# Performance work log

Hardware: AMD Instinct MI355X
Metric: run time of the kernel (lower is better)

Reference implementation:

```python
import jax, jax.numpy as jnp
import numpy as np

ROPE_BASE = 100.0  # CroCo/InfiniteVGGT-style 2D RoPE base

def _rope_1d(sub, pos, base=ROPE_BASE):
    # sub: (B,H,N,half), pos: (B,N) float
    half = sub.shape[-1]
    quarter = half // 2
    inv_freq = 1.0 / (base ** (jnp.arange(quarter, dtype=jnp.float32) / quarter))
    ang = pos[:, None, :, None] * inv_freq  # (B,1,N,quarter)
    cos, sin = jnp.cos(ang), jnp.sin(ang)
    x1, x2 = sub[..., :quarter], sub[..., quarter:]
    return jnp.concatenate([x1 * cos - x2 * sin, x1 * sin + x2 * cos], axis=-1)

def rope_2d(t, positions):
    # t: (B,H,N,Dh); positions: (B,N,2) int (y,x)
    Dh = t.shape[-1]
    half = Dh // 2
    pos_f = positions.astype(t.dtype)
    y = _rope_1d(t[..., :half], pos_f[..., 0])
    x = _rope_1d(t[..., half:], pos_f[..., 1])
    return jnp.concatenate([y, x], axis=-1)

def setup_inputs() -> dict:
    key = jax.random.key(0)
    k1, k2, k3, k4 = jax.random.split(key, 4)
    B, N, C, H = 2, 2048, 1024, 16
    x = jax.random.normal(k1, (B, N, C), dtype=jnp.float32)
    positions = jax.random.randint(k2, (B, N, 2), 0, 64, dtype=jnp.int32)
    qkv_w = jax.random.normal(k3, (3 * C, C), dtype=jnp.float32) * (C ** -0.5)
    proj_w = jax.random.normal(k4, (C, C), dtype=jnp.float32) * (C ** -0.5)
    proj_b = jnp.zeros((C,), dtype=jnp.float32)
    return {"x": x, "positions": positions, "qkv_w": qkv_w, "proj_w": proj_w, "proj_b": proj_b}

def reference(x, positions, qkv_w, proj_w, proj_b):
    B, N, C = x.shape
    H = 16
    Dh = C // H
    scale = Dh ** -0.5
    qkv = (x @ qkv_w.T).reshape(B, N, 3, H, Dh).transpose(2, 0, 3, 1, 4)  # (3,B,H,N,Dh)
    q, k, v = qkv[0], qkv[1], qkv[2]
    q = rope_2d(q, positions)
    k = rope_2d(k, positions)
    attn = jnp.einsum('bhnd,bhmd->bhnm', q, k) * scale  # (B,H,N,N)
    attn = jax.nn.softmax(attn, axis=-1)
    out = jnp.einsum('bhnm,bhmd->bhnd', attn, v)  # (B,H,N,Dh)
    out = out.transpose(0, 2, 1, 3).reshape(B, N, C)
    return out @ proj_w.T + proj_b
```

## Files before the change

### kernel.cpp

```cpp
#include <hip/hip_runtime.h>
#include <cmath>

typedef unsigned short u16;
typedef unsigned int   u32;
typedef __attribute__((ext_vector_type(8))) __bf16 bf16x8;
typedef __attribute__((ext_vector_type(2))) __bf16 bf16x2;
typedef __attribute__((ext_vector_type(4))) float  f32x4;

constexpr int BB = 2, SEQ = 2048, CH = 1024, NH = 16, DH = 64;

__device__ inline u16 f2bf(float f) {
    u32 u = __builtin_bit_cast(u32, f);
    u += 0x7FFF + ((u >> 16) & 1);
    return (u16)(u >> 16);
}
__device__ inline float bf2f(u16 b) { return __builtin_bit_cast(float, (u32)b << 16); }
__device__ inline u32 pkbf(float a, float b) {
#if __has_builtin(__builtin_amdgcn_cvt_pk_bf16_f32)
    bf16x2 r = __builtin_amdgcn_cvt_pk_bf16_f32(a, b);
    return __builtin_bit_cast(u32, r);
#else
    return (u32)f2bf(a) | ((u32)f2bf(b) << 16);
#endif
}
__device__ inline float fexp2(float x) {
#if __has_builtin(__builtin_amdgcn_exp2f)
    return __builtin_amdgcn_exp2f(x);
#else
    return exp2f(x);
#endif
}

__device__ inline void gld_lds16(const void* g, void* l) {
    __builtin_amdgcn_global_load_lds((const __attribute__((address_space(1))) void*)g,
                                     (__attribute__((address_space(3))) void*)l, 16, 0, 0);
}
__device__ inline f32x4 mfma16(bf16x8 a, bf16x8 b, f32x4 c) {
    return __builtin_amdgcn_mfma_f32_16x16x32_bf16(a, b, c, 0, 0, 0);
}
__device__ inline bf16x8 ld_frag(const u16* p) {
    return __builtin_bit_cast(bf16x8, *(const uint4*)p);
}

__global__ __launch_bounds__(256) void convert_kernel(const float* __restrict__ x,
                                                      const float* __restrict__ wq,
                                                      const float* __restrict__ wp,
                                                      u16* __restrict__ xb,
                                                      u16* __restrict__ wqb,
                                                      u16* __restrict__ wpb,
                                                      float2* __restrict__ tabq,
                                                      float2* __restrict__ tabk) {
    const int q = blockIdx.x * 256 + threadIdx.x;
    if (q >= 2097152) {
        const int idx = q - 2097152;
        if (idx < 1024) {
            const int p = idx >> 4, i = idx & 15;
            const float f = exp2f(-(float)i * 0.41524101186092f);
            float s, c;
            sincosf((float)p * f, &s, &c);
            tabk[idx] = make_float2(c, s);
            tabq[idx] = make_float2(c * 0.18033688011112042f,
                                    s * 0.18033688011112042f);
        }
        return;
    }
    const float* src; u16* dst; int idx;
    if (q < 1048576)            { src = x;  dst = xb;  idx = q; }
    else if (q < 1048576+786432){ src = wq; dst = wqb; idx = q - 1048576; }
    else                        { src = wp; dst = wpb; idx = q - 1048576 - 786432; }
    float4 v = *(const float4*)(src + (size_t)idx * 4);
    ushort4 o; o.x = f2bf(v.x); o.y = f2bf(v.y); o.z = f2bf(v.z); o.w = f2bf(v.w);
    *(ushort4*)(dst + (size_t)idx * 4) = o;
}

__global__ __launch_bounds__(256) void gemm_qkv_rope(const u16* __restrict__ A,
                                                     const u16* __restrict__ Bw,
                                                     const int* __restrict__ pos,
                                                     const float2* __restrict__ tabq,
                                                     const float2* __restrict__ tabk,
                                                     u16* __restrict__ Qb,
                                                     u16* __restrict__ Kb,
                                                     u16* __restrict__ Vt) {
    __shared__ u16 smem[18432];
    const int t = threadIdx.x, lane = t & 63, w = t >> 6;
    const int l15 = lane & 15, quad = lane >> 4;
    const int wm = w >> 1, wn = w & 1;
    const int m0 = blockIdx.y * 128, n0 = blockIdx.x * 128;
    const int K = CH;

    const int row0 = t >> 2, v0 = t & 3;
    const int gi0 = (v0 - (row0 >> 1)) & 3;
    const int row1 = row0 + 64;
    const int gi1 = (v0 - (row1 >> 1)) & 3;

    const u16* A0 = A  + (size_t)(m0 + row0) * K + gi0 * 8;
    const u16* A1 = A  + (size_t)(m0 + row1) * K + gi1 * 8;
    const u16* B0 = Bw + (size_t)(n0 + row0) * K + gi0 * 8;
    const u16* B1 = Bw + (size_t)(n0 + row1) * K + gi1 * 8;

    gld_lds16(A0, smem + t * 8);
    gld_lds16(A1, smem + 2048 + t * 8);
    gld_lds16(B0, smem + 8192 + t * 8);
    gld_lds16(B1, smem + 10240 + t * 8);

    f32x4 acc[4][4] = {};
    for (int kt = 0; kt < K / 32; ++kt) {
        __syncthreads();
        const int cur = (kt & 1) * 4096;
        if (kt + 1 < K / 32) {
            const int off = (kt + 1) * 32;
            const int nxt = ((kt + 1) & 1) * 4096;
            gld_lds16(A0 + off, smem + nxt + t * 8);
            gld_lds16(A1 + off, smem + nxt + 2048 + t * 8);
            gld_lds16(B0 + off, smem + 8192 + nxt + t * 8);
            gld_lds16(B1 + off, smem + 8192 + nxt + 2048 + t * 8);
        }
        const u16* as = smem + cur;
        const u16* bs = smem + 8192 + cur;
        bf16x8 af[4], bfv[4];
#pragma unroll
        for (int mi = 0; mi < 4; ++mi) {
            const int r = wm * 64 + mi * 16 + l15;
            af[mi] = ld_frag(as + (r * 4 + ((quad + (r >> 1)) & 3)) * 8);
        }
#pragma unroll
        for (int nj = 0; nj < 4; ++nj) {
            const int r = wn * 64 + nj * 16 + l15;
            bfv[nj] = ld_frag(bs + (r * 4 + ((quad + (r >> 1)) & 3)) * 8);
        }
#pragma unroll
        for (int mi = 0; mi < 4; ++mi)
#pragma unroll
            for (int nj = 0; nj < 4; ++nj)
                acc[mi][nj] = mfma16(af[mi], bfv[nj], acc[mi][nj]);
    }

    const int reg = n0 >> 10;
    const int h   = ((n0 & 1023) >> 6) + wn;
    if (reg < 2) {
        const float2* tab = reg ? tabk : tabq;
        u16* dst = reg ? Kb : Qb;
#pragma unroll
        for (int mi = 0; mi < 4; ++mi) {
#pragma unroll
            for (int r = 0; r < 4; ++r) {
                const int m = m0 + wm * 64 + mi * 16 + quad * 4 + r;
                const int bh = (m >> 11) * NH + h;
                const int n  = m & 2047;
                const int2 pp = *(const int2*)(pos + m * 2);
                const float2 ty = tab[pp.x * 16 + l15];
                const float2 tx = tab[pp.y * 16 + l15];
                const float x1 = acc[mi][0][r], x2 = acc[mi][1][r];
                const float y1 = acc[mi][2][r], y2 = acc[mi][3][r];
                u16* p = dst + ((size_t)bh * SEQ + n) * 64 + l15;
                p[0]  = f2bf(x1 * ty.x - x2 * ty.y);
                p[16] = f2bf(x1 * ty.y + x2 * ty.x);
                p[32] = f2bf(y1 * tx.x - y2 * tx.y);
                p[48] = f2bf(y1 * tx.y + y2 * tx.x);
            }
        }
    } else {
        __syncthreads();
        u16* T = smem + w * 4608;
#pragma unroll
        for (int mi = 0; mi < 4; ++mi)
#pragma unroll
            for (int nj = 0; nj < 4; ++nj)
#pragma unroll
                for (int r = 0; r < 4; ++r)
                    T[(nj * 16 + l15) * 72 + mi * 16 + quad * 4 + r] =
                        f2bf(acc[mi][nj][r]);
        const int bh = (m0 >> 11) * NH + h;
        const int nbase = (m0 & 2047) + wm * 64;
        u16* gdst = Vt + ((size_t)bh * 64 + lane) * SEQ + nbase;
#pragma unroll
        for (int j = 0; j < 8; ++j)
            *(uint4*)(gdst + j * 8) = *(const uint4*)(T + lane * 72 + j * 8);
    }
}

__global__ __launch_bounds__(256) void gemm_bf16(const u16* __restrict__ A,
                                                 const u16* __restrict__ Bw,
                                                 const float* __restrict__ bias,
                                                 float* __restrict__ C,
                                                 int M, int N, int K) {
    __shared__ u16 smem[16384];
    const int t = threadIdx.x, lane = t & 63, w = t >> 6;
    const int l15 = lane & 15, quad = lane >> 4;
    const int wm = w >> 1, wn = w & 1;
    const int m0 = blockIdx.y * 128, n0 = blockIdx.x * 128;

    const int row0 = t >> 2, v0 = t & 3;
    const int gi0 = (v0 - (row0 >> 1)) & 3;
    const int row1 = row0 + 64;
    const int gi1 = (v0 - (row1 >> 1)) & 3;

    const u16* A0 = A  + (size_t)(m0 + row0) * K + gi0 * 8;
    const u16* A1 = A  + (size_t)(m0 + row1) * K + gi1 * 8;
    const u16* B0 = Bw + (size_t)(n0 + row0) * K + gi0 * 8;
    const u16* B1 = Bw + (size_t)(n0 + row1) * K + gi1 * 8;

    gld_lds16(A0, smem + t * 8);
    gld_lds16(A1, smem + 2048 + t * 8);
    gld_lds16(B0, smem + 8192 + t * 8);
    gld_lds16(B1, smem + 10240 + t * 8);

    f32x4 acc[4][4] = {};
    for (int kt = 0; kt < K / 32; ++kt) {
        __syncthreads();
        const int cur = (kt & 1) * 4096;
        if (kt + 1 < K / 32) {
            const int off = (kt + 1) * 32;
            const int nxt = ((kt + 1) & 1) * 4096;
            gld_lds16(A0 + off, smem + nxt + t * 8);
            gld_lds16(A1 + off, smem + nxt + 2048 + t * 8);
            gld_lds16(B0 + off, smem + 8192 + nxt + t * 8);
            gld_lds16(B1 + off, smem + 8192 + nxt + 2048 + t * 8);
        }
        const u16* as = smem + cur;
        const u16* bs = smem + 8192 + cur;
        bf16x8 af[4], bfv[4];
#pragma unroll
        for (int mi = 0; mi < 4; ++mi) {
            const int r = wm * 64 + mi * 16 + l15;
            af[mi] = ld_frag(as + (r * 4 + ((quad + (r >> 1)) & 3)) * 8);
        }
#pragma unroll
        for (int nj = 0; nj < 4; ++nj) {
            const int r = wn * 64 + nj * 16 + l15;
            bfv[nj] = ld_frag(bs + (r * 4 + ((quad + (r >> 1)) & 3)) * 8);
        }
#pragma unroll
        for (int mi = 0; mi < 4; ++mi)
#pragma unroll
            for (int nj = 0; nj < 4; ++nj)
                acc[mi][nj] = mfma16(af[mi], bfv[nj], acc[mi][nj]);
    }
#pragma unroll
    for (int mi = 0; mi < 4; ++mi)
#pragma unroll
        for (int nj = 0; nj < 4; ++nj) {
            const int n = n0 + wn * 64 + nj * 16 + l15;
            const float bv = bias[n];
#pragma unroll
            for (int r = 0; r < 4; ++r) {
                const int m = m0 + wm * 64 + mi * 16 + quad * 4 + r;
                C[(size_t)m * N + n] = acc[mi][nj][r] + bv;
            }
        }
}

__global__ __launch_bounds__(256, 4) void attn_mfma(const u16* __restrict__ Qb,
                                                    const u16* __restrict__ Kb,
                                                    const u16* __restrict__ Vt,
                                                    u16* __restrict__ Opart,
                                                    float* __restrict__ lpart) {
    __shared__ u16 Ks[64 * 64];
    __shared__ u16 Vs[64 * 64];
    __shared__ u16 Ps[128 * 72];
    const int t = threadIdx.x, lane = t & 63, w = t >> 6;
    const int l15 = lane & 15, quad = lane >> 4;
    const int bh = blockIdx.y;
    const int q0 = blockIdx.x * 128;
    const int z  = blockIdx.z;

    const int rowA = t >> 3, vA = t & 7;
    const int giA = (vA - rowA) & 7;
    const int rowB = rowA + 32;
    const int giB = (vA - rowB) & 7;

    const size_t kbase = (size_t)bh * SEQ * 64;
    const size_t vbase = (size_t)bh * 64 * SEQ;

    const uint4 ones_u = {0x3F803F80u, 0x3F803F80u, 0x3F803F80u, 0x3F803F80u};
    const bf16x8 onesf = __builtin_bit_cast(bf16x8, ones_u);

    bf16x8 aq[2][2];
#pragma unroll
    for (int mi = 0; mi < 2; ++mi)
#pragma unroll
        for (int ks = 0; ks < 2; ++ks)
            aq[mi][ks] = ld_frag(Qb + ((size_t)bh * SEQ + q0 + w * 32 + mi * 16 + l15) * 64
                                 + ks * 32 + quad * 8);

    f32x4 oacc[2][4] = {};
    f32x4 lacc[2] = {};

    for (int kt = 0; kt < 16; ++kt) {
        const int k0 = z * 1024 + kt * 64;
        __syncthreads();
        gld_lds16(Kb + kbase + (size_t)(k0 + rowA) * 64 + giA * 8, Ks + t * 8);
        gld_lds16(Kb + kbase + (size_t)(k0 + rowB) * 64 + giB * 8, Ks + 2048 + t * 8);
        gld_lds16(Vt + vbase + (size_t)rowA * SEQ + k0 + giA * 8, Vs + t * 8);
        gld_lds16(Vt + vbase + (size_t)rowB * SEQ + k0 + giB * 8, Vs + 2048 + t * 8);
        __syncthreads();

        f32x4 sacc[2][4] = {};
#pragma unroll
        for (int ks = 0; ks < 2; ++ks)
#pragma unroll
            for (int nk = 0; nk < 4; ++nk) {
                const int rK = nk * 16 + l15;
                const bf16x8 kf = ld_frag(Ks + (rK * 8 + (((ks * 4 + quad) + rK) & 7)) * 8);
                sacc[0][nk] = mfma16(kf, aq[0][ks], sacc[0][nk]);
                sacc[1][nk] = mfma16(kf, aq[1][ks], sacc[1][nk]);
            }

#pragma unroll
        for (int mi = 0; mi < 2; ++mi) {
            const int prow = (w * 32 + mi * 16 + l15) * 72;
#pragma unroll
            for (int nk = 0; nk < 4; ++nk) {
                const float p0 = fexp2(sacc[mi][nk][0]);
                const float p1 = fexp2(sacc[mi][nk][1]);
                const float p2 = fexp2(sacc[mi][nk][2]);
                const float p3 = fexp2(sacc[mi][nk][3]);
                uint2 pk; pk.x = pkbf(p0, p1); pk.y = pkbf(p2, p3);
                *(uint2*)&Ps[prow + nk * 16 + quad * 4] = pk;
            }
        }

#pragma unroll
        for (int ks = 0; ks < 2; ++ks) {
            const bf16x8 ap0 = ld_frag(Ps + (w * 32 + l15) * 72 + ks * 32 + quad * 8);
            const bf16x8 ap1 = ld_frag(Ps + (w * 32 + 16 + l15) * 72 + ks * 32 + quad * 8);
            lacc[0] = mfma16(ap0, onesf, lacc[0]);
            lacc[1] = mfma16(ap1, onesf, lacc[1]);
#pragma unroll
            for (int nj = 0; nj < 4; ++nj) {
                const int rV = nj * 16 + l15;
                const bf16x8 vf = ld_frag(Vs + (rV * 8 + (((ks * 4 + quad) + rV) & 7)) * 8);
                oacc[0][nj] = mfma16(ap0, vf, oacc[0][nj]);
                oacc[1][nj] = mfma16(ap1, vf, oacc[1][nj]);
            }
        }
    }

#pragma unroll
    for (int mi = 0; mi < 2; ++mi)
#pragma unroll
        for (int r = 0; r < 4; ++r) {
            const int qrow = q0 + w * 32 + mi * 16 + quad * 4 + r;
            if (l15 == 0)
                lpart[((size_t)z * 32 + bh) * SEQ + qrow] = lacc[mi][r];
            const size_t orow = (((size_t)z * 32 + bh) * SEQ + qrow) * 64;
#pragma unroll
            for (int nj = 0; nj < 4; ++nj)
                Opart[orow + nj * 16 + l15] = f2bf(oacc[mi][nj][r]);
        }
}

__global__ __launch_bounds__(256) void merge_kernel(const u16* __restrict__ Opart,
                                                    const float* __restrict__ lpart,
                                                    u16* __restrict__ Ob) {
    const int gid = blockIdx.x * 256 + threadIdx.x;
    const int d4 = gid & 15, q = (gid >> 4) & 2047, bh = gid >> 15;
    const size_t i1 = ((size_t)bh * SEQ + q) * 64 + d4 * 4;
    const size_t i2 = i1 + (size_t)32 * SEQ * 64;
    const float inv = 1.0f / (lpart[(size_t)bh * SEQ + q] +
                              lpart[(size_t)(32 + bh) * SEQ + q]);
    const ushort4 a = *(const ushort4*)(Opart + i1);
    const ushort4 b = *(const ushort4*)(Opart + i2);
    ushort4 o;
    o.x = f2bf((bf2f(a.x) + bf2f(b.x)) * inv);
    o.y = f2bf((bf2f(a.y) + bf2f(b.y)) * inv);
    o.z = f2bf((bf2f(a.z) + bf2f(b.z)) * inv);
    o.w = f2bf((bf2f(a.w) + bf2f(b.w)) * inv);
    const int b_ = bh >> 4, h = bh & 15;
    *(ushort4*)(Ob + ((size_t)(b_ * SEQ + q)) * CH + h * 64 + d4 * 4) = o;
}

extern "C" void kernel_launch(void* const* d_in, const int* in_sizes, int n_in,
                              void* d_out, int out_size, void* d_ws, size_t ws_size,
                              hipStream_t stream) {
    const float* x      = (const float*)d_in[0];
    const int*   pos    = (const int*)d_in[1];
    const float* qkv_w  = (const float*)d_in[2];
    const float* proj_w = (const float*)d_in[3];
    const float* proj_b = (const float*)d_in[4];
    float* out = (float*)d_out;

    u16* ws = (u16*)d_ws;
    u16* x_bf    = ws;
    u16* attn_bf = ws;
    u16* wq_bf   = ws + 4194304;
    float* lpart = (float*)(ws + 4194304);
    u16* wp_bf   = ws + 7340032;
    u16* Qb      = ws + 8388608;
    u16* Kb      = ws + 12582912;
    u16* Vt      = ws + 16777216;
    u16* Opart   = ws + 20971520;
    float2* tabq = (float2*)(ws + 20971520);
    float2* tabk = (float2*)(ws + 20971520 + 4096);

    const int M = BB * SEQ;

    convert_kernel<<<8196, 256, 0, stream>>>(x, qkv_w, proj_w, x_bf, wq_bf, wp_bf,
                                             tabq, tabk);
    gemm_qkv_rope<<<dim3(3 * CH / 128, M / 128), 256, 0, stream>>>(
        x_bf, wq_bf, pos, tabq, tabk, Qb, Kb, Vt);
    attn_mfma<<<dim3(SEQ / 128, BB * NH, 2), 256, 0, stream>>>(Qb, Kb, Vt, Opart, lpart);
    merge_kernel<<<4096, 256, 0, stream>>>(Opart, lpart, attn_bf);
    gemm_bf16<<<dim3(CH / 128, M / 128), 256, 0, stream>>>(
        attn_bf, wp_bf, proj_b, out, M, CH, CH);
}
```

Baseline: 201.6 us.

## Drop attention split-K merge, double-buffer KV, split-K proj GEMM with atomics

The QKV GEMM epilogue now stages RoPE'd Q/K through LDS and writes coalesced 16-byte rows, and V's transpose store is remapped so lanes write contiguous chunks. Attention no longer splits the key range in two. Each block walks all 2048 keys with double-buffered K/V LDS tiles, normalises in-kernel and writes the final bf16 output directly. This removes the merge kernel and the partial-output traffic, but halves the attention grid and drops the occupancy hint. The projection GEMM is split into two K halves that accumulate into a zero-initialised output with float atomics. This adds parallelism at the cost of a memset and atomic traffic.

```diff
diff --git a/kernel.cpp b/kernel.cpp
--- a/kernel.cpp
+++ b/kernel.cpp
@@ -137,31 +137,39 @@
 
     const int reg = n0 >> 10;
     const int h   = ((n0 & 1023) >> 6) + wn;
+    __syncthreads();
+    u16* T = smem + w * 4608;
+    const int rsel = lane >> 3, csel = lane & 7;
     if (reg < 2) {
         const float2* tab = reg ? tabk : tabq;
-        u16* dst = reg ? Kb : Qb;
+        u16* dstb = reg ? Kb : Qb;
 #pragma unroll
         for (int mi = 0; mi < 4; ++mi) {
 #pragma unroll
             for (int r = 0; r < 4; ++r) {
                 const int m = m0 + wm * 64 + mi * 16 + quad * 4 + r;
-                const int bh = (m >> 11) * NH + h;
-                const int n  = m & 2047;
                 const int2 pp = *(const int2*)(pos + m * 2);
                 const float2 ty = tab[pp.x * 16 + l15];
                 const float2 tx = tab[pp.y * 16 + l15];
                 const float x1 = acc[mi][0][r], x2 = acc[mi][1][r];
                 const float y1 = acc[mi][2][r], y2 = acc[mi][3][r];
-                u16* p = dst + ((size_t)bh * SEQ + n) * 64 + l15;
-                p[0]  = f2bf(x1 * ty.x - x2 * ty.y);
-                p[16] = f2bf(x1 * ty.y + x2 * ty.x);
-                p[32] = f2bf(y1 * tx.x - y2 * tx.y);
-                p[48] = f2bf(y1 * tx.y + y2 * tx.x);
+                const int ml = (mi * 16 + quad * 4 + r) * 72;
+                T[ml + l15]      = f2bf(x1 * ty.x - x2 * ty.y);
+                T[ml + l15 + 16] = f2bf(x1 * ty.y + x2 * ty.x);
+                T[ml + l15 + 32] = f2bf(y1 * tx.x - y2 * tx.y);
+                T[ml + l15 + 48] = f2bf(y1 * tx.y + y2 * tx.x);
             }
         }
+        const int mbase = m0 + wm * 64;
+        const int bh = (mbase >> 11) * NH + h;
+        const int nbase = mbase & 2047;
+#pragma unroll
+        for (int j = 0; j < 8; ++j) {
+            const int row = rsel + j * 8;
+            u16* gp = dstb + ((size_t)bh * SEQ + nbase + row) * 64 + csel * 8;
+            *(uint4*)gp = *(const uint4*)&T[row * 72 + csel * 8];
+        }
     } else {
-        __syncthreads();
-        u16* T = smem + w * 4608;
 #pragma unroll
         for (int mi = 0; mi < 4; ++mi)
 #pragma unroll
@@ -172,105 +180,36 @@
                         f2bf(acc[mi][nj][r]);
         const int bh = (m0 >> 11) * NH + h;
         const int nbase = (m0 & 2047) + wm * 64;
-        u16* gdst = Vt + ((size_t)bh * 64 + lane) * SEQ + nbase;
-#pragma unroll
-        for (int j = 0; j < 8; ++j)
-            *(uint4*)(gdst + j * 8) = *(const uint4*)(T + lane * 72 + j * 8);
+#pragma unroll
+        for (int j = 0; j < 8; ++j) {
+            const int d = rsel + j * 8;
+            u16* gp = Vt + ((size_t)bh * 64 + d) * SEQ + nbase + csel * 8;
+            *(uint4*)gp = *(const uint4*)&T[d * 72 + csel * 8];
+        }
     }
 }
 
-__global__ __launch_bounds__(256) void gemm_bf16(const u16* __restrict__ A,
-                                                 const u16* __restrict__ Bw,
-                                                 const float* __restrict__ bias,
-                                                 float* __restrict__ C,
-                                                 int M, int N, int K) {
-    __shared__ u16 smem[16384];
-    const int t = threadIdx.x, lane = t & 63, w = t >> 6;
-    const int l15 = lane & 15, quad = lane >> 4;
-    const int wm = w >> 1, wn = w & 1;
-    const int m0 = blockIdx.y * 128, n0 = blockIdx.x * 128;
-
-    const int row0 = t >> 2, v0 = t & 3;
-    const int gi0 = (v0 - (row0 >> 1)) & 3;
-    const int row1 = row0 + 64;
-    const int gi1 = (v0 - (row1 >> 1)) & 3;
-
-    const u16* A0 = A  + (size_t)(m0 + row0) * K + gi0 * 8;
-    const u16* A1 = A  + (size_t)(m0 + row1) * K + gi1 * 8;
-    const u16* B0 = Bw + (size_t)(n0 + row0) * K + gi0 * 8;
-    const u16* B1 = Bw + (size_t)(n0 + row1) * K + gi1 * 8;
-
-    gld_lds16(A0, smem + t * 8);
-    gld_lds16(A1, smem + 2048 + t * 8);
-    gld_lds16(B0, smem + 8192 + t * 8);
-    gld_lds16(B1, smem + 10240 + t * 8);
-
-    f32x4 acc[4][4] = {};
-    for (int kt = 0; kt < K / 32; ++kt) {
-        __syncthreads();
-        const int cur = (kt & 1) * 4096;
-        if (kt + 1 < K / 32) {
-            const int off = (kt + 1) * 32;
-            const int nxt = ((kt + 1) & 1) * 4096;
-            gld_lds16(A0 + off, smem + nxt + t * 8);
-            gld_lds16(A1 + off, smem + nxt + 2048 + t * 8);
-            gld_lds16(B0 + off, smem + 8192 + nxt + t * 8);
-            gld_lds16(B1 + off, smem + 8192 + nxt + 2048 + t * 8);
-        }
-        const u16* as = smem + cur;
-        const u16* bs = smem + 8192 + cur;
-        bf16x8 af[4], bfv[4];
-#pragma unroll
-        for (int mi = 0; mi < 4; ++mi) {
-            const int r = wm * 64 + mi * 16 + l15;
-            af[mi] = ld_frag(as + (r * 4 + ((quad + (r >> 1)) & 3)) * 8);
-        }
-#pragma unroll
-        for (int nj = 0; nj < 4; ++nj) {
-            const int r = wn * 64 + nj * 16 + l15;
-            bfv[nj] = ld_frag(bs + (r * 4 + ((quad + (r >> 1)) & 3)) * 8);
-        }
-#pragma unroll
-        for (int mi = 0; mi < 4; ++mi)
-#pragma unroll
-            for (int nj = 0; nj < 4; ++nj)
-                acc[mi][nj] = mfma16(af[mi], bfv[nj], acc[mi][nj]);
-    }
-#pragma unroll
-    for (int mi = 0; mi < 4; ++mi)
-#pragma unroll
-        for (int nj = 0; nj < 4; ++nj) {
-            const int n = n0 + wn * 64 + nj * 16 + l15;
-            const float bv = bias[n];
-#pragma unroll
-            for (int r = 0; r < 4; ++r) {
-                const int m = m0 + wm * 64 + mi * 16 + quad * 4 + r;
-                C[(size_t)m * N + n] = acc[mi][nj][r] + bv;
-            }
-        }
-}
-
-__global__ __launch_bounds__(256, 4) void attn_mfma(const u16* __restrict__ Qb,
-                                                    const u16* __restrict__ Kb,
-                                                    const u16* __restrict__ Vt,
-                                                    u16* __restrict__ Opart,
-                                                    float* __restrict__ lpart) {
-    __shared__ u16 Ks[64 * 64];
-    __shared__ u16 Vs[64 * 64];
+__global__ __launch_bounds__(256) void attn_mfma(const u16* __restrict__ Qb,
+                                                 const u16* __restrict__ Kb,
+                                                 const u16* __restrict__ Vt,
+                                                 u16* __restrict__ Ob) {
+    __shared__ u16 Ks[2][4096];
+    __shared__ u16 Vs[2][4096];
     __shared__ u16 Ps[128 * 72];
     const int t = threadIdx.x, lane = t & 63, w = t >> 6;
     const int l15 = lane & 15, quad = lane >> 4;
     const int bh = blockIdx.y;
     const int q0 = blockIdx.x * 128;
-    const int z  = blockIdx.z;
 
     const int rowA = t >> 3, vA = t & 7;
     const int giA = (vA - rowA) & 7;
     const int rowB = rowA + 32;
     const int giB = (vA - rowB) & 7;
 
-    const size_t kbase = (size_t)bh * SEQ * 64;
-    const size_t vbase = (size_t)bh * 64 * SEQ;
+    const u16* Ksrc0 = Kb + (size_t)bh * SEQ * 64 + (size_t)rowA * 64 + giA * 8;
+    const u16* Ksrc1 = Kb + (size_t)bh * SEQ * 64 + (size_t)rowB * 64 + giB * 8;
+    const u16* Vsrc0 = Vt + (size_t)bh * 64 * SEQ + (size_t)rowA * SEQ + giA * 8;
+    const u16* Vsrc1 = Vt + (size_t)bh * 64 * SEQ + (size_t)rowB * SEQ + giB * 8;
 
     const uint4 ones_u = {0x3F803F80u, 0x3F803F80u, 0x3F803F80u, 0x3F803F80u};
     const bf16x8 onesf = __builtin_bit_cast(bf16x8, ones_u);
@@ -286,14 +225,21 @@
     f32x4 oacc[2][4] = {};
     f32x4 lacc[2] = {};
 
-    for (int kt = 0; kt < 16; ++kt) {
-        const int k0 = z * 1024 + kt * 64;
+    gld_lds16(Ksrc0, &Ks[0][t * 8]);
+    gld_lds16(Ksrc1, &Ks[0][t * 8 + 2048]);
+    gld_lds16(Vsrc0, &Vs[0][t * 8]);
+    gld_lds16(Vsrc1, &Vs[0][t * 8 + 2048]);
+
+    for (int kt = 0; kt < 32; ++kt) {
         __syncthreads();
-        gld_lds16(Kb + kbase + (size_t)(k0 + rowA) * 64 + giA * 8, Ks + t * 8);
-        gld_lds16(Kb + kbase + (size_t)(k0 + rowB) * 64 + giB * 8, Ks + 2048 + t * 8);
-        gld_lds16(Vt + vbase + (size_t)rowA * SEQ + k0 + giA * 8, Vs + t * 8);
-        gld_lds16(Vt + vbase + (size_t)rowB * SEQ + k0 + giB * 8, Vs + 2048 + t * 8);
-        __syncthreads();
+        const int cur = kt & 1;
+        if (kt + 1 < 32) {
+            const int nxt = cur ^ 1;
+            gld_lds16(Ksrc0 + (kt + 1) * 4096, &Ks[nxt][t * 8]);
+            gld_lds16(Ksrc1 + (kt + 1) * 4096, &Ks[nxt][t * 8 + 2048]);
+            gld_lds16(Vsrc0 + (kt + 1) * 64,   &Vs[nxt][t * 8]);
+            gld_lds16(Vsrc1 + (kt + 1) * 64,   &Vs[nxt][t * 8 + 2048]);
+        }
 
         f32x4 sacc[2][4] = {};
 #pragma unroll
@@ -301,7 +247,8 @@
 #pragma unroll
             for (int nk = 0; nk < 4; ++nk) {
                 const int rK = nk * 16 + l15;
-                const bf16x8 kf = ld_frag(Ks + (rK * 8 + (((ks * 4 + quad) + rK) & 7)) * 8);
+                const bf16x8 kf =
+                    ld_frag(&Ks[cur][(rK * 8 + (((ks * 4 + quad) + rK) & 7)) * 8]);
                 sacc[0][nk] = mfma16(kf, aq[0][ks], sacc[0][nk]);
                 sacc[1][nk] = mfma16(kf, aq[1][ks], sacc[1][nk]);
             }
@@ -322,52 +269,106 @@
 
 #pragma unroll
         for (int ks = 0; ks < 2; ++ks) {
-            const bf16x8 ap0 = ld_frag(Ps + (w * 32 + l15) * 72 + ks * 32 + quad * 8);
-            const bf16x8 ap1 = ld_frag(Ps + (w * 32 + 16 + l15) * 72 + ks * 32 + quad * 8);
+            const bf16x8 ap0 = ld_frag(&Ps[(w * 32 + l15) * 72 + ks * 32 + quad * 8]);
+            const bf16x8 ap1 = ld_frag(&Ps[(w * 32 + 16 + l15) * 72 + ks * 32 + quad * 8]);
             lacc[0] = mfma16(ap0, onesf, lacc[0]);
             lacc[1] = mfma16(ap1, onesf, lacc[1]);
 #pragma unroll
             for (int nj = 0; nj < 4; ++nj) {
                 const int rV = nj * 16 + l15;
-                const bf16x8 vf = ld_frag(Vs + (rV * 8 + (((ks * 4 + quad) + rV) & 7)) * 8);
+                const bf16x8 vf =
+                    ld_frag(&Vs[cur][(rV * 8 + (((ks * 4 + quad) + rV) & 7)) * 8]);
                 oacc[0][nj] = mfma16(ap0, vf, oacc[0][nj]);
                 oacc[1][nj] = mfma16(ap1, vf, oacc[1][nj]);
             }
         }
     }
 
+    const int b_ = bh >> 4, h = bh & 15;
 #pragma unroll
     for (int mi = 0; mi < 2; ++mi)
 #pragma unroll
         for (int r = 0; r < 4; ++r) {
+            const float inv = 1.0f / lacc[mi][r];
             const int qrow = q0 + w * 32 + mi * 16 + quad * 4 + r;
-            if (l15 == 0)
-                lpart[((size_t)z * 32 + bh) * SEQ + qrow] = lacc[mi][r];
-            const size_t orow = (((size_t)z * 32 + bh) * SEQ + qrow) * 64;
+            u16* op = Ob + ((size_t)(b_ * SEQ + qrow)) * CH + h * 64;
 #pragma unroll
             for (int nj = 0; nj < 4; ++nj)
-                Opart[orow + nj * 16 + l15] = f2bf(oacc[mi][nj][r]);
-        }
-}
-
-__global__ __launch_bounds__(256) void merge_kernel(const u16* __restrict__ Opart,
-                                                    const float* __restrict__ lpart,
-                                                    u16* __restrict__ Ob) {
-    const int gid = blockIdx.x * 256 + threadIdx.x;
-    const int d4 = gid & 15, q = (gid >> 4) & 2047, bh = gid >> 15;
-    const size_t i1 = ((size_t)bh * SEQ + q) * 64 + d4 * 4;
-    const size_t i2 = i1 + (size_t)32 * SEQ * 64;
-    const float inv = 1.0f / (lpart[(size_t)bh * SEQ + q] +
-                              lpart[(size_t)(32 + bh) * SEQ + q]);
-    const ushort4 a = *(const ushort4*)(Opart + i1);
-    const ushort4 b = *(const ushort4*)(Opart + i2);
-    ushort4 o;
-    o.x = f2bf((bf2f(a.x) + bf2f(b.x)) * inv);
-    o.y = f2bf((bf2f(a.y) + bf2f(b.y)) * inv);
-    o.z = f2bf((bf2f(a.z) + bf2f(b.z)) * inv);
-    o.w = f2bf((bf2f(a.w) + bf2f(b.w)) * inv);
-    const int b_ = bh >> 4, h = bh & 15;
-    *(ushort4*)(Ob + ((size_t)(b_ * SEQ + q)) * CH + h * 64 + d4 * 4) = o;
+                op[nj * 16 + l15] = f2bf(oacc[mi][nj][r] * inv);
+        }
+}
+
+__global__ __launch_bounds__(256) void gemm_proj(const u16* __restrict__ A,
+                                                 const u16* __restrict__ Bw,
+                                                 const float* __restrict__ bias,
+                                                 float* __restrict__ C) {
+    __shared__ u16 smem[16384];
+    const int t = threadIdx.x, lane = t & 63, w = t >> 6;
+    const int l15 = lane & 15, quad = lane >> 4;
+    const int wm = w >> 1, wn = w & 1;
+    const int m0 = blockIdx.y * 128, n0 = blockIdx.x * 128;
+    const int K = CH, N = CH;
+    const int k0 = blockIdx.z * 512;
+
+    const int row0 = t >> 2, v0 = t & 3;
+    const int gi0 = (v0 - (row0 >> 1)) & 3;
+    const int row1 = row0 + 64;
+    const int gi1 = (v0 - (row1 >> 1)) & 3;
+
+    const u16* A0 = A  + (size_t)(m0 + row0) * K + k0 + gi0 * 8;
+    const u16* A1 = A  + (size_t)(m0 + row1) * K + k0 + gi1 * 8;
+    const u16* B0 = Bw + (size_t)(n0 + row0) * K + k0 + gi0 * 8;
+    const u16* B1 = Bw + (size_t)(n0 + row1) * K + k0 + gi1 * 8;
+
+    gld_lds16(A0, smem + t * 8);
+    gld_lds16(A1, smem + 2048 + t * 8);
+    gld_lds16(B0, smem + 8192 + t * 8);
+    gld_lds16(B1, smem + 10240 + t * 8);
+
+    f32x4 acc[4][4] = {};
+    for (int kt = 0; kt < 16; ++kt) {
+        __syncthreads();
+        const int cur = (kt & 1) * 4096;
+        if (kt + 1 < 16) {
+            const int off = (kt + 1) * 32;
+            const int nxt = ((kt + 1) & 1) * 4096;
+            gld_lds16(A0 + off, smem + nxt + t * 8);
+            gld_lds16(A1 + off, smem + nxt + 2048 + t * 8);
+            gld_lds16(B0 + off, smem + 8192 + nxt + t * 8);
+            gld_lds16(B1 + off, smem + 8192 + nxt + 2048 + t * 8);
+        }
+        const u16* as = smem + cur;
+        const u16* bs = smem + 8192 + cur;
+        bf16x8 af[4], bfv[4];
+#pragma unroll
+        for (int mi = 0; mi < 4; ++mi) {
+            const int r = wm * 64 + mi * 16 + l15;
+            af[mi] = ld_frag(as + (r * 4 + ((quad + (r >> 1)) & 3)) * 8);
+        }
+#pragma unroll
+        for (int nj = 0; nj < 4; ++nj) {
+            const int r = wn * 64 + nj * 16 + l15;
+            bfv[nj] = ld_frag(bs + (r * 4 + ((quad + (r >> 1)) & 3)) * 8);
+        }
+#pragma unroll
+        for (int mi = 0; mi < 4; ++mi)
+#pragma unroll
+            for (int nj = 0; nj < 4; ++nj)
+                acc[mi][nj] = mfma16(af[mi], bfv[nj], acc[mi][nj]);
+    }
+    const int addb = (blockIdx.z == 0);
+#pragma unroll
+    for (int mi = 0; mi < 4; ++mi)
+#pragma unroll
+        for (int nj = 0; nj < 4; ++nj) {
+            const int n = n0 + wn * 64 + nj * 16 + l15;
+            const float bv = addb ? bias[n] : 0.0f;
+#pragma unroll
+            for (int r = 0; r < 4; ++r) {
+                const int m = m0 + wm * 64 + mi * 16 + quad * 4 + r;
+                atomicAdd(&C[(size_t)m * N + n], acc[mi][nj][r] + bv);
+            }
+        }
 }
 
 extern "C" void kernel_launch(void* const* d_in, const int* in_sizes, int n_in,
@@ -384,23 +385,21 @@
     u16* x_bf    = ws;
     u16* attn_bf = ws;
     u16* wq_bf   = ws + 4194304;
-    float* lpart = (float*)(ws + 4194304);
     u16* wp_bf   = ws + 7340032;
     u16* Qb      = ws + 8388608;
     u16* Kb      = ws + 12582912;
     u16* Vt      = ws + 16777216;
-    u16* Opart   = ws + 20971520;
     float2* tabq = (float2*)(ws + 20971520);
     float2* tabk = (float2*)(ws + 20971520 + 4096);
 
     const int M = BB * SEQ;
 
+    hipMemsetAsync(out, 0, (size_t)out_size * sizeof(float), stream);
     convert_kernel<<<8196, 256, 0, stream>>>(x, qkv_w, proj_w, x_bf, wq_bf, wp_bf,
                                              tabq, tabk);
     gemm_qkv_rope<<<dim3(3 * CH / 128, M / 128), 256, 0, stream>>>(
         x_bf, wq_bf, pos, tabq, tabk, Qb, Kb, Vt);
-    attn_mfma<<<dim3(SEQ / 128, BB * NH, 2), 256, 0, stream>>>(Qb, Kb, Vt, Opart, lpart);
-    merge_kernel<<<4096, 256, 0, stream>>>(Opart, lpart, attn_bf);
-    gemm_bf16<<<dim3(CH / 128, M / 128), 256, 0, stream>>>(
-        attn_bf, wp_bf, proj_b, out, M, CH, CH);
-}
+    attn_mfma<<<dim3(SEQ / 128, BB * NH), 256, 0, stream>>>(Qb, Kb, Vt, attn_bf);
+    gemm_proj<<<dim3(CH / 128, M / 128, 2), 256, 0, stream>>>(
+        attn_bf, wp_bf, proj_b, out);
+}
```

After: 226.3 us. 12.3% more time.
